# Kernel optimization log

Measured on AMD Instinct MI355X. Metric: run time of the kernel, lower is better.

The kernel has to match this reference:

```python
import jax, jax.numpy as jnp
import numpy as np

B, L, M = 64, 2048, 128  # trees, leaves per complete binary tree, mem_dim (== in_dim)


def setup_inputs() -> dict:
    key = jax.random.key(0)
    ks = jax.random.split(key, 16)
    n = lambda k, s, sc=1.0: jax.random.normal(k, s, dtype=jnp.float32) * sc
    W = 0.08  # small init scale for gate weights
    return {
        "embs": n(ks[0], (B, L, M)),
        "root_c": n(ks[1], (B, M)),
        "root_h": n(ks[2], (B, M)),
        "Wi": n(ks[3], (M, M), W), "bi": jnp.zeros((M,), jnp.float32),
        "Wf": n(ks[4], (M, M), W), "bf": jnp.zeros((M,), jnp.float32),
        "Wu": n(ks[5], (M, M), W), "bu": jnp.zeros((M,), jnp.float32),
        "Wc": n(ks[6], (M, M), W), "bc": jnp.zeros((M,), jnp.float32),
        "Wo": n(ks[7], (M, M), W), "bo": jnp.zeros((M,), jnp.float32),
    }


def reference(embs, root_c, root_h, Wi, bi, Wf, bf, Wu, bu, Wc, bc, Wo, bo):
    # Top-down binary-tree LSTM over B complete binary trees, vectorized per level.
    Bn, Ln, Mn = embs.shape
    depth = int(np.log2(Ln))  # root at level 0, leaves at level `depth`

    def composer(pc, ph):
        # BinaryTreeTopDownComposer: gates from parent hidden, cell mixes parent cell
        i = jax.nn.sigmoid(ph @ Wi + bi)
        pf = jax.nn.sigmoid(ph @ Wf + bf)
        u = jnp.tanh(ph @ Wu + bu)
        c = i * u + pf * pc
        return c, jnp.tanh(c)

    def leaf(x):
        # BinaryTreeLeafModule
        c = x @ Wc + bc
        o = jax.nn.sigmoid(x @ Wo + bo)
        return c, o * jnp.tanh(c)

    # root state comes from bp_lstm.root_c / root_h
    pc, ph = root_c[:, None, :], root_h[:, None, :]  # [B, 1, M]
    for _ in range(1, depth):  # internal levels: each node composed from its parent
        pc2 = jnp.repeat(pc, 2, axis=1)  # broadcast parent state to both children
        ph2 = jnp.repeat(ph, 2, axis=1)
        pc, ph = composer(pc2, ph2)

    # leaf level: state = cat(leaf(emb), leaf(parent_h), leaf(parent_c)) along features
    pcl = jnp.repeat(pc, 2, axis=1)  # [B, L, M]
    phl = jnp.repeat(ph, 2, axis=1)
    ce, he = leaf(embs)
    cph, hph = leaf(phl)
    cpc, hpc = leaf(pcl)
    c_leaf = jnp.concatenate([ce, cph, cpc], axis=-1)  # [B, L, 3M]
    h_leaf = jnp.concatenate([he, hph, hpc], axis=-1)  # [B, L, 3M]
    return jnp.concatenate([c_leaf, h_leaf], axis=-1)  # [B, L, 6M]
```

## Files before the change

### kernel.cpp

```cpp
#include <hip/hip_runtime.h>
#include <cstdint>
#include <cstddef>

#define Bb   64
#define Ll   2048
#define Mm   128
#define ROWS (Bb * Ll)
#define OUTC 768
#define LDA  136
#define LDF  132

typedef __attribute__((ext_vector_type(4))) float  f32x4;
typedef __attribute__((ext_vector_type(8))) short  bf16x8;
typedef __attribute__((ext_vector_type(4))) short  short4v;
typedef __bf16 bf16x8b __attribute__((ext_vector_type(8)));

__device__ __forceinline__ float rcp_(float x) {
#if __has_builtin(__builtin_amdgcn_rcpf)
    return __builtin_amdgcn_rcpf(x);
#else
    return 1.0f / x;
#endif
}
__device__ __forceinline__ float sigmoid_(float x) {
    return rcp_(1.0f + __expf(-x));
}
__device__ __forceinline__ float tanh_(float x) {
    float ax = fabsf(x);
    float r  = __expf(-2.0f * ax);
    float t  = (1.0f - r) * rcp_(1.0f + r);
    return x < 0.0f ? -t : t;
}
__device__ __forceinline__ short f2bf(float f) {
    uint32_t u = __builtin_bit_cast(uint32_t, f);
    u = (u + 0x7FFFu + ((u >> 16) & 1u)) >> 16;
    return (short)(u & 0xFFFFu);
}


__global__ __launch_bounds__(128)
void state_kernel(const float* __restrict__ root_c, const float* __restrict__ root_h,
                  const float* __restrict__ Wi, const float* __restrict__ bi,
                  const float* __restrict__ Wf, const float* __restrict__ bfv,
                  const float* __restrict__ Wu, const float* __restrict__ bu,
                  const float* __restrict__ Wc, const float* __restrict__ bc,
                  const float* __restrict__ Wo, const float* __restrict__ bo,
                  float* __restrict__ ws, short* __restrict__ wbf)
{
    const int b = blockIdx.x;
    const int m = threadIdx.x;
    __shared__ float h_sh[Mm];
    __shared__ float c_sh[Mm];

    {
        int gtid = b * 128 + m;
        #pragma unroll
        for (int j = 0; j < 4; ++j) {
            int idx  = gtid + 8192 * j;
            int gate = idx >> 14;
            int col  = (idx >> 7) & 127;
            int k    = idx & 127;
            const float* W = gate ? Wo : Wc;
            wbf[idx] = f2bf(W[k * Mm + col]);
        }
    }

    float c = root_c[b * Mm + m];
    h_sh[m] = root_h[b * Mm + m];
    __syncthreads();

    const float bi_m = bi[m], bf_m = bfv[m], bu_m = bu[m];

    for (int it = 0; it < 10; ++it) {
        float di0 = 0.f, df0 = 0.f, du0 = 0.f;
        float di1 = 0.f, df1 = 0.f, du1 = 0.f;
        #pragma unroll 8
        for (int k = 0; k < Mm; k += 2) {
            float h0 = h_sh[k], h1 = h_sh[k + 1];
            di0 = fmaf(h0, Wi[k * Mm + m], di0);
            di1 = fmaf(h1, Wi[(k + 1) * Mm + m], di1);
            df0 = fmaf(h0, Wf[k * Mm + m], df0);
            df1 = fmaf(h1, Wf[(k + 1) * Mm + m], df1);
            du0 = fmaf(h0, Wu[k * Mm + m], du0);
            du1 = fmaf(h1, Wu[(k + 1) * Mm + m], du1);
        }
        float ig = sigmoid_(di0 + di1 + bi_m);
        float fg = sigmoid_(df0 + df1 + bf_m);
        float ug = tanh_(du0 + du1 + bu_m);
        c = ig * ug + fg * c;
        __syncthreads();
        h_sh[m] = tanh_(c);
        __syncthreads();
    }

    c_sh[m] = c;
    __syncthreads();

    float dch = 0.f, doh = 0.f, dcc = 0.f, doc = 0.f;
    #pragma unroll 8
    for (int k = 0; k < Mm; ++k) {
        float hk = h_sh[k], ck = c_sh[k];
        float wc = Wc[k * Mm + m], wo = Wo[k * Mm + m];
        dch = fmaf(hk, wc, dch);
        doh = fmaf(hk, wo, doh);
        dcc = fmaf(ck, wc, dcc);
        doc = fmaf(ck, wo, doc);
    }
    const float bcm = bc[m], bom = bo[m];
    float cph = dch + bcm;
    float cpc = dcc + bcm;
    float hph = sigmoid_(doh + bom) * tanh_(cph);
    float hpc = sigmoid_(doc + bom) * tanh_(cpc);

    ws[0 * Bb * Mm + b * Mm + m] = cph;
    ws[1 * Bb * Mm + b * Mm + m] = cpc;
    ws[2 * Bb * Mm + b * Mm + m] = hph;
    ws[3 * Bb * Mm + b * Mm + m] = hpc;
}

__global__ __launch_bounds__(512, 4)
void fused_kernel(const float* __restrict__ embs,
                  const short* __restrict__ wbf,
                  const float* __restrict__ bc, const float* __restrict__ bo,
                  const float* __restrict__ state,
                  float* __restrict__ out)
{
    __shared__ __align__(16) char smem[35840];
    short* A_sh = (short*)smem;
    float* ce_l = (float*)smem;
    float* he_l = (float*)(smem + 16896);
    float* st_l = (float*)(smem + 33792);

    const int tid  = threadIdx.x;
    const int w    = tid >> 6;
    const int lane = tid & 63;
    const int g    = lane >> 4;
    const int ln   = lane & 15;
    const int n0   = w * 16 + ln;
    const int rowbase = blockIdx.x * 64;
    const int b       = rowbase >> 11;

    bf16x8 bfrag[2][4];
    #pragma unroll
    for (int gate = 0; gate < 2; ++gate)
        #pragma unroll
        for (int ks = 0; ks < 4; ++ks)
            bfrag[gate][ks] = *(const bf16x8*)(
                wbf + gate * (Mm * Mm) + n0 * Mm + ks * 32 + g * 8);

    const float biasc = bc[n0];
    const float biaso = bo[n0];

    st_l[tid] = state[(tid >> 7) * (Bb * Mm) + b * Mm + (tid & 127)];

    #pragma unroll
    for (int i = 0; i < 4; ++i) {
        int idx = tid + 512 * i;
        int r   = idx >> 5;
        int kq  = idx & 31;
        f32x4 v = *(const f32x4*)(embs + (size_t)(rowbase + r) * Mm + kq * 4);
        short4v s4;
        s4[0] = f2bf(v[0]); s4[1] = f2bf(v[1]);
        s4[2] = f2bf(v[2]); s4[3] = f2bf(v[3]);
        *(short4v*)(&A_sh[r * LDA + kq * 4]) = s4;
    }
    __syncthreads();

    f32x4 acc[4][2];
    #pragma unroll
    for (int rt = 0; rt < 4; ++rt)
        #pragma unroll
        for (int gate = 0; gate < 2; ++gate) {
            float bv = gate ? biaso : biasc;
            acc[rt][gate][0] = bv; acc[rt][gate][1] = bv;
            acc[rt][gate][2] = bv; acc[rt][gate][3] = bv;
        }

    #pragma unroll
    for (int ks = 0; ks < 4; ++ks) {
        bf16x8 af[4];
        #pragma unroll
        for (int rt = 0; rt < 4; ++rt)
            af[rt] = *(const bf16x8*)(&A_sh[(rt * 16 + ln) * LDA + ks * 32 + g * 8]);
        #pragma unroll
        for (int rt = 0; rt < 4; ++rt)
            #pragma unroll
            for (int gate = 0; gate < 2; ++gate)
                acc[rt][gate] = __builtin_amdgcn_mfma_f32_16x16x32_bf16(
                    __builtin_bit_cast(bf16x8b, af[rt]),
                    __builtin_bit_cast(bf16x8b, bfrag[gate][ks]),
                    acc[rt][gate], 0, 0, 0);
    }
    __syncthreads();

    #pragma unroll
    for (int half = 0; half < 2; ++half) {
        #pragma unroll
        for (int q = 0; q < 2; ++q) {
            int rt = half * 2 + q;
            #pragma unroll
            for (int r = 0; r < 4; ++r) {
                int rowL = q * 16 + g * 4 + r;
                float cv = acc[rt][0][r];
                float hv = sigmoid_(acc[rt][1][r]) * tanh_(cv);
                ce_l[rowL * LDF + n0] = cv;
                he_l[rowL * LDF + n0] = hv;
            }
        }
        __syncthreads();

        #pragma unroll
        for (int i = 0; i < 12; ++i) {
            int u  = tid + 512 * i;
            int rg = u / 192;
            int s  = u - rg * 192;
            int sec = s >> 5;
            int c   = s & 31;
            const float* src =
                (sec == 0) ? (ce_l + rg * LDF + c * 4) :
                (sec == 3) ? (he_l + rg * LDF + c * 4) :
                (st_l + ((sec < 3) ? (sec - 1) : (sec - 2)) * 128 + c * 4);
            f32x4 v = *(const f32x4*)src;
            *(f32x4*)(out + (size_t)(rowbase + half * 32 + rg) * OUTC + s * 4) = v;
        }
        if (half == 0) __syncthreads();
    }
}

extern "C" void kernel_launch(void* const* d_in, const int* in_sizes, int n_in,
                              void* d_out, int out_size, void* d_ws, size_t ws_size,
                              hipStream_t stream) {
    const float* embs   = (const float*)d_in[0];
    const float* root_c = (const float*)d_in[1];
    const float* root_h = (const float*)d_in[2];
    const float* Wi = (const float*)d_in[3];
    const float* bi = (const float*)d_in[4];
    const float* Wf = (const float*)d_in[5];
    const float* bfv= (const float*)d_in[6];
    const float* Wu = (const float*)d_in[7];
    const float* bu = (const float*)d_in[8];
    const float* Wc = (const float*)d_in[9];
    const float* bc = (const float*)d_in[10];
    const float* Wo = (const float*)d_in[11];
    const float* bo = (const float*)d_in[12];

    float* out   = (float*)d_out;
    float* state = (float*)d_ws;
    short* wbf   = (short*)d_ws + 65536;

    state_kernel<<<dim3(Bb), dim3(Mm), 0, stream>>>(
        root_c, root_h, Wi, bi, Wf, bfv, Wu, bu, Wc, bc, Wo, bo, state, wbf);
    fused_kernel<<<dim3(2048), dim3(512), 0, stream>>>(
        embs, wbf, bc, bo, state, out);
}
```

Baseline: 132.4 us.

## Split state recurrence over K and double-buffer two row tiles per block

The state kernel now uses 512 threads, splitting each 128-long dot product into four K-chunks and reducing them through shared memory. This shortens the serial 10-level recurrence per block. The fused kernel processes two 64-row tiles per block with two LDS buffers, so the second tile's embedding load is issued before the first tile's MFMA and epilogue, and uses nontemporal loads. The cost is doubled shared memory (about 69KB), which may lower occupancy below the 4 blocks per CU the launch bounds ask for, plus extra barriers.

```diff
diff --git a/kernel.cpp b/kernel.cpp
--- a/kernel.cpp
+++ b/kernel.cpp
@@ -38,7 +38,7 @@
 }
 
 
-__global__ __launch_bounds__(128)
+__global__ __launch_bounds__(512)
 void state_kernel(const float* __restrict__ root_c, const float* __restrict__ root_h,
                   const float* __restrict__ Wi, const float* __restrict__ bi,
                   const float* __restrict__ Wf, const float* __restrict__ bfv,
@@ -47,35 +47,39 @@
                   const float* __restrict__ Wo, const float* __restrict__ bo,
                   float* __restrict__ ws, short* __restrict__ wbf)
 {
-    const int b = blockIdx.x;
-    const int m = threadIdx.x;
+    const int b   = blockIdx.x;
+    const int tid = threadIdx.x;
+    const int m   = tid & 127;
+    const int q   = tid >> 7;
+    const int k0  = q * 32;
+
     __shared__ float h_sh[Mm];
     __shared__ float c_sh[Mm];
+    __shared__ float part[4][4][Mm];
 
     {
-        int gtid = b * 128 + m;
-        #pragma unroll
-        for (int j = 0; j < 4; ++j) {
-            int idx  = gtid + 8192 * j;
-            int gate = idx >> 14;
-            int col  = (idx >> 7) & 127;
-            int k    = idx & 127;
-            const float* W = gate ? Wo : Wc;
-            wbf[idx] = f2bf(W[k * Mm + col]);
-        }
-    }
-
-    float c = root_c[b * Mm + m];
-    h_sh[m] = root_h[b * Mm + m];
+        int idx  = b * 512 + tid;
+        int gate = idx >> 14;
+        int col  = (idx >> 7) & 127;
+        int k    = idx & 127;
+        const float* W = gate ? Wo : Wc;
+        wbf[idx] = f2bf(W[k * Mm + col]);
+    }
+
+    float c = 0.f;
+    if (q == 0) {
+        c = root_c[b * Mm + m];
+        h_sh[m] = root_h[b * Mm + m];
+    }
     __syncthreads();
 
     const float bi_m = bi[m], bf_m = bfv[m], bu_m = bu[m];
 
     for (int it = 0; it < 10; ++it) {
-        float di0 = 0.f, df0 = 0.f, du0 = 0.f;
-        float di1 = 0.f, df1 = 0.f, du1 = 0.f;
-        #pragma unroll 8
-        for (int k = 0; k < Mm; k += 2) {
+        float di0 = 0.f, di1 = 0.f, df0 = 0.f, df1 = 0.f, du0 = 0.f, du1 = 0.f;
+        #pragma unroll
+        for (int kk = 0; kk < 32; kk += 2) {
+            int k = k0 + kk;
             float h0 = h_sh[k], h1 = h_sh[k + 1];
             di0 = fmaf(h0, Wi[k * Mm + m], di0);
             di1 = fmaf(h1, Wi[(k + 1) * Mm + m], di1);
@@ -84,21 +88,29 @@
             du0 = fmaf(h0, Wu[k * Mm + m], du0);
             du1 = fmaf(h1, Wu[(k + 1) * Mm + m], du1);
         }
-        float ig = sigmoid_(di0 + di1 + bi_m);
-        float fg = sigmoid_(df0 + df1 + bf_m);
-        float ug = tanh_(du0 + du1 + bu_m);
-        c = ig * ug + fg * c;
+        part[0][q][m] = di0 + di1;
+        part[1][q][m] = df0 + df1;
+        part[2][q][m] = du0 + du1;
         __syncthreads();
-        h_sh[m] = tanh_(c);
+        if (q == 0) {
+            float di = (part[0][0][m] + part[0][1][m]) + (part[0][2][m] + part[0][3][m]);
+            float df = (part[1][0][m] + part[1][1][m]) + (part[1][2][m] + part[1][3][m]);
+            float du = (part[2][0][m] + part[2][1][m]) + (part[2][2][m] + part[2][3][m]);
+            float ig = sigmoid_(di + bi_m);
+            float fg = sigmoid_(df + bf_m);
+            float ug = tanh_(du + bu_m);
+            c = ig * ug + fg * c;
+            h_sh[m] = tanh_(c);
+        }
         __syncthreads();
     }
-
-    c_sh[m] = c;
+    if (q == 0) c_sh[m] = c;
     __syncthreads();
 
     float dch = 0.f, doh = 0.f, dcc = 0.f, doc = 0.f;
-    #pragma unroll 8
-    for (int k = 0; k < Mm; ++k) {
+    #pragma unroll
+    for (int kk = 0; kk < 32; ++kk) {
+        int k = k0 + kk;
         float hk = h_sh[k], ck = c_sh[k];
         float wc = Wc[k * Mm + m], wo = Wo[k * Mm + m];
         dch = fmaf(hk, wc, dch);
@@ -106,16 +118,26 @@
         dcc = fmaf(ck, wc, dcc);
         doc = fmaf(ck, wo, doc);
     }
-    const float bcm = bc[m], bom = bo[m];
-    float cph = dch + bcm;
-    float cpc = dcc + bcm;
-    float hph = sigmoid_(doh + bom) * tanh_(cph);
-    float hpc = sigmoid_(doc + bom) * tanh_(cpc);
-
-    ws[0 * Bb * Mm + b * Mm + m] = cph;
-    ws[1 * Bb * Mm + b * Mm + m] = cpc;
-    ws[2 * Bb * Mm + b * Mm + m] = hph;
-    ws[3 * Bb * Mm + b * Mm + m] = hpc;
+    part[0][q][m] = dch;
+    part[1][q][m] = doh;
+    part[2][q][m] = dcc;
+    part[3][q][m] = doc;
+    __syncthreads();
+    if (q == 0) {
+        float Dch = (part[0][0][m] + part[0][1][m]) + (part[0][2][m] + part[0][3][m]);
+        float Doh = (part[1][0][m] + part[1][1][m]) + (part[1][2][m] + part[1][3][m]);
+        float Dcc = (part[2][0][m] + part[2][1][m]) + (part[2][2][m] + part[2][3][m]);
+        float Doc = (part[3][0][m] + part[3][1][m]) + (part[3][2][m] + part[3][3][m]);
+        const float bcm = bc[m], bom = bo[m];
+        float cph = Dch + bcm;
+        float cpc = Dcc + bcm;
+        float hph = sigmoid_(Doh + bom) * tanh_(cph);
+        float hpc = sigmoid_(Doc + bom) * tanh_(cpc);
+        ws[0 * Bb * Mm + b * Mm + m] = cph;
+        ws[1 * Bb * Mm + b * Mm + m] = cpc;
+        ws[2 * Bb * Mm + b * Mm + m] = hph;
+        ws[3 * Bb * Mm + b * Mm + m] = hpc;
+    }
 }
 
 __global__ __launch_bounds__(512, 4)
@@ -125,11 +147,12 @@
                   const float* __restrict__ state,
                   float* __restrict__ out)
 {
-    __shared__ __align__(16) char smem[35840];
-    short* A_sh = (short*)smem;
-    float* ce_l = (float*)smem;
-    float* he_l = (float*)(smem + 16896);
-    float* st_l = (float*)(smem + 33792);
+    __shared__ __align__(16) char smem[70656];
+    short* A0   = (short*)smem;
+    short* A1   = (short*)(smem + 17408);
+    float* ce_l = (float*)(smem + 34816);
+    float* he_l = (float*)(smem + 51712);
+    float* st_l = (float*)(smem + 68608);
 
     const int tid  = threadIdx.x;
     const int w    = tid >> 6;
@@ -137,8 +160,9 @@
     const int g    = lane >> 4;
     const int ln   = lane & 15;
     const int n0   = w * 16 + ln;
-    const int rowbase = blockIdx.x * 64;
-    const int b       = rowbase >> 11;
+    const int rowbase0 = blockIdx.x * 128;
+    const int rowbase1 = rowbase0 + 64;
+    const int b        = rowbase0 >> 11;
 
     bf16x8 bfrag[2][4];
     #pragma unroll
@@ -147,84 +171,107 @@
         for (int ks = 0; ks < 4; ++ks)
             bfrag[gate][ks] = *(const bf16x8*)(
                 wbf + gate * (Mm * Mm) + n0 * Mm + ks * 32 + g * 8);
-
     const float biasc = bc[n0];
     const float biaso = bo[n0];
-
     st_l[tid] = state[(tid >> 7) * (Bb * Mm) + b * Mm + (tid & 127)];
 
-    #pragma unroll
-    for (int i = 0; i < 4; ++i) {
-        int idx = tid + 512 * i;
-        int r   = idx >> 5;
-        int kq  = idx & 31;
-        f32x4 v = *(const f32x4*)(embs + (size_t)(rowbase + r) * Mm + kq * 4);
-        short4v s4;
-        s4[0] = f2bf(v[0]); s4[1] = f2bf(v[1]);
-        s4[2] = f2bf(v[2]); s4[3] = f2bf(v[3]);
-        *(short4v*)(&A_sh[r * LDA + kq * 4]) = s4;
-    }
-    __syncthreads();
-
+    auto stage_load = [&](int rowbase, f32x4 (&r)[4]) {
+        #pragma unroll
+        for (int i = 0; i < 4; ++i) {
+            int idx = tid + 512 * i;
+            int rr  = idx >> 5;
+            int kq  = idx & 31;
+            r[i] = __builtin_nontemporal_load(
+                (const f32x4*)(embs + (size_t)(rowbase + rr) * Mm + kq * 4));
+        }
+    };
+    auto stage_write = [&](short* A, const f32x4 (&r)[4]) {
+        #pragma unroll
+        for (int i = 0; i < 4; ++i) {
+            int idx = tid + 512 * i;
+            int rr  = idx >> 5;
+            int kq  = idx & 31;
+            short4v s4;
+            s4[0] = f2bf(r[i][0]); s4[1] = f2bf(r[i][1]);
+            s4[2] = f2bf(r[i][2]); s4[3] = f2bf(r[i][3]);
+            *(short4v*)(&A[rr * LDA + kq * 4]) = s4;
+        }
+    };
+    auto do_mfma = [&](const short* A, f32x4 (&acc)[4][2]) {
+        #pragma unroll
+        for (int rt = 0; rt < 4; ++rt)
+            #pragma unroll
+            for (int gate = 0; gate < 2; ++gate) {
+                float bv = gate ? biaso : biasc;
+                acc[rt][gate][0] = bv; acc[rt][gate][1] = bv;
+                acc[rt][gate][2] = bv; acc[rt][gate][3] = bv;
+            }
+        #pragma unroll
+        for (int ks = 0; ks < 4; ++ks) {
+            bf16x8 af[4];
+            #pragma unroll
+            for (int rt = 0; rt < 4; ++rt)
+                af[rt] = *(const bf16x8*)(&A[(rt * 16 + ln) * LDA + ks * 32 + g * 8]);
+            #pragma unroll
+            for (int rt = 0; rt < 4; ++rt)
+                #pragma unroll
+                for (int gate = 0; gate < 2; ++gate)
+                    acc[rt][gate] = __builtin_amdgcn_mfma_f32_16x16x32_bf16(
+                        __builtin_bit_cast(bf16x8b, af[rt]),
+                        __builtin_bit_cast(bf16x8b, bfrag[gate][ks]),
+                        acc[rt][gate], 0, 0, 0);
+        }
+    };
+    auto epilogue = [&](int rowbase, f32x4 (&acc)[4][2]) {
+        #pragma unroll
+        for (int half = 0; half < 2; ++half) {
+            #pragma unroll
+            for (int qq = 0; qq < 2; ++qq) {
+                int rt = half * 2 + qq;
+                #pragma unroll
+                for (int r = 0; r < 4; ++r) {
+                    int rowL = qq * 16 + g * 4 + r;
+                    float cv = acc[rt][0][r];
+                    float hv = sigmoid_(acc[rt][1][r]) * tanh_(cv);
+                    ce_l[rowL * LDF + n0] = cv;
+                    he_l[rowL * LDF + n0] = hv;
+                }
+            }
+            __syncthreads();
+            #pragma unroll
+            for (int i = 0; i < 12; ++i) {
+                int u  = tid + 512 * i;
+                int rg = u / 192;
+                int s  = u - rg * 192;
+                int sec = s >> 5;
+                int cc  = s & 31;
+                const float* src =
+                    (sec == 0) ? (ce_l + rg * LDF + cc * 4) :
+                    (sec == 3) ? (he_l + rg * LDF + cc * 4) :
+                    (st_l + ((sec < 3) ? (sec - 1) : (sec - 2)) * 128 + cc * 4);
+                f32x4 v = *(const f32x4*)src;
+                *(f32x4*)(out + (size_t)(rowbase + half * 32 + rg) * OUTC + s * 4) = v;
+            }
+            __syncthreads();
+        }
+    };
+
+    f32x4 r0[4], r1[4];
     f32x4 acc[4][2];
-    #pragma unroll
-    for (int rt = 0; rt < 4; ++rt)
-        #pragma unroll
-        for (int gate = 0; gate < 2; ++gate) {
-            float bv = gate ? biaso : biasc;
-            acc[rt][gate][0] = bv; acc[rt][gate][1] = bv;
-            acc[rt][gate][2] = bv; acc[rt][gate][3] = bv;
-        }
-
-    #pragma unroll
-    for (int ks = 0; ks < 4; ++ks) {
-        bf16x8 af[4];
-        #pragma unroll
-        for (int rt = 0; rt < 4; ++rt)
-            af[rt] = *(const bf16x8*)(&A_sh[(rt * 16 + ln) * LDA + ks * 32 + g * 8]);
-        #pragma unroll
-        for (int rt = 0; rt < 4; ++rt)
-            #pragma unroll
-            for (int gate = 0; gate < 2; ++gate)
-                acc[rt][gate] = __builtin_amdgcn_mfma_f32_16x16x32_bf16(
-                    __builtin_bit_cast(bf16x8b, af[rt]),
-                    __builtin_bit_cast(bf16x8b, bfrag[gate][ks]),
-                    acc[rt][gate], 0, 0, 0);
-    }
-    __syncthreads();
-
-    #pragma unroll
-    for (int half = 0; half < 2; ++half) {
-        #pragma unroll
-        for (int q = 0; q < 2; ++q) {
-            int rt = half * 2 + q;
-            #pragma unroll
-            for (int r = 0; r < 4; ++r) {
-                int rowL = q * 16 + g * 4 + r;
-                float cv = acc[rt][0][r];
-                float hv = sigmoid_(acc[rt][1][r]) * tanh_(cv);
-                ce_l[rowL * LDF + n0] = cv;
-                he_l[rowL * LDF + n0] = hv;
-            }
-        }
-        __syncthreads();
-
-        #pragma unroll
-        for (int i = 0; i < 12; ++i) {
-            int u  = tid + 512 * i;
-            int rg = u / 192;
-            int s  = u - rg * 192;
-            int sec = s >> 5;
-            int c   = s & 31;
-            const float* src =
-                (sec == 0) ? (ce_l + rg * LDF + c * 4) :
-                (sec == 3) ? (he_l + rg * LDF + c * 4) :
-                (st_l + ((sec < 3) ? (sec - 1) : (sec - 2)) * 128 + c * 4);
-            f32x4 v = *(const f32x4*)src;
-            *(f32x4*)(out + (size_t)(rowbase + half * 32 + rg) * OUTC + s * 4) = v;
-        }
-        if (half == 0) __syncthreads();
-    }
+
+    stage_load(rowbase0, r0);
+    stage_write(A0, r0);
+    __syncthreads();
+
+    stage_load(rowbase1, r1);
+
+    do_mfma(A0, acc);
+    stage_write(A1, r1);
+    __syncthreads();
+
+    epilogue(rowbase0, acc);
+    do_mfma(A1, acc);
+    epilogue(rowbase1, acc);
 }
 
 extern "C" void kernel_launch(void* const* d_in, const int* in_sizes, int n_in,
@@ -248,8 +295,8 @@
     float* state = (float*)d_ws;
     short* wbf   = (short*)d_ws + 65536;
 
-    state_kernel<<<dim3(Bb), dim3(Mm), 0, stream>>>(
+    state_kernel<<<dim3(Bb), dim3(512), 0, stream>>>(
         root_c, root_h, Wi, bi, Wf, bfv, Wu, bu, Wc, bc, Wo, bo, state, wbf);
-    fused_kernel<<<dim3(2048), dim3(512), 0, stream>>>(
+    fused_kernel<<<dim3(1024), dim3(512), 0, stream>>>(
         embs, wbf, bc, bo, state, out);
 }
```

After: 110.4 us. 16.6% less time.
